# Performance work log

Hardware: AMD Instinct MI355X
Metric: run time of the kernel (lower is better)

The kernel has to match this reference:

```python
import jax, jax.numpy as jnp
import numpy as np

HIDDEN = 1024
FFN = 3584
NUM_EXPERTS = 8
TOP_K = 2
B, S = 2, 1024


def setup_inputs() -> dict:
    key = jax.random.key(0)
    k0, k1, k2, k3 = jax.random.split(key, 4)
    hidden_states = jax.random.normal(k0, (B, S, HIDDEN), dtype=jnp.float32)
    # torch Linear stores [out, in]; we keep gate as [E, H] (matches nn.Linear weight)
    gate_w = jax.random.normal(k1, (NUM_EXPERTS, HIDDEN), dtype=jnp.float32) * 0.02
    # GroupedLinear weights stored as [E, in, out] for direct x @ W per expert
    w_gate_up = jax.random.normal(k2, (NUM_EXPERTS, HIDDEN, 2 * FFN), dtype=jnp.float32) * 0.02
    w_down = jax.random.normal(k3, (NUM_EXPERTS, FFN, HIDDEN), dtype=jnp.float32) * 0.02
    return {"hidden_states": hidden_states, "gate_w": gate_w,
            "w_gate_up": w_gate_up, "w_down": w_down}


def reference(hidden_states, gate_w, w_gate_up, w_down):
    b, s, h = hidden_states.shape
    x = hidden_states.reshape(-1, h)                      # [T, H]
    T = x.shape[0]
    E = gate_w.shape[0]

    # Router: logits -> fp32 softmax -> top-k -> renormalize (Mixtral semantics)
    router_logits = x @ gate_w.T                          # [T, E]
    probs = jax.nn.softmax(router_logits.astype(jnp.float32), axis=-1)
    top_vals, top_idx = jax.lax.top_k(probs, TOP_K)       # [T, K]
    top_vals = top_vals / top_vals.sum(axis=-1, keepdims=True)
    top_vals = top_vals.astype(x.dtype)

    # Dense combine weights [T, E]: scatter top-k probs to expert slots.
    # Equivalent to permute -> grouped GEMM -> unpermute-with-probs.
    combine = jnp.zeros((T, E), dtype=x.dtype).at[
        jnp.arange(T)[:, None], top_idx].add(top_vals)

    out = jnp.zeros_like(x)
    for e in range(E):  # fixed small expert count
        gu = x @ w_gate_up[e]                             # [T, 2F]
        gate_proj, up_proj = jnp.split(gu, 2, axis=-1)
        act = jax.nn.silu(gate_proj) * up_proj            # [T, F]
        out = out + combine[:, e:e + 1] * (act @ w_down[e])

    return out.reshape(b, s, h), router_logits
```

## Files before the change

kernel.cpp:

```cpp
#include <hip/hip_runtime.h>
#include <hip/hip_bf16.h>
#include <stdint.h>

#define HIDDEN  1024
#define FFN     3584
#define NE      8
#define NTOK    2048
#define CAP     2048
#define OUT_ELEMS (NTOK * HIDDEN)

#define X_OFF   0u
#define CNT_OFF (4u*1024u*1024u)
#define TOK_OFF (CNT_OFF + 256u)
#define WGT_OFF (TOK_OFF + 65536u)
#define ACT_OFF (WGT_OFF + 65536u)
#define ACT_SZ  (4096u * 3584u * 2u)
#define WGU_OFF (ACT_OFF + ACT_SZ)
#define WGU_SZ  (8u*56u*16u*16384u)
#define WDB_OFF (WGU_OFF + WGU_SZ)
#define WDB_SZ  (8u*8u*56u*16384u)
#define WS_NEED ((size_t)WDB_OFF + (size_t)WDB_SZ)

typedef __attribute__((ext_vector_type(8))) short short8;
typedef __attribute__((ext_vector_type(4))) float floatx4;

static __device__ __forceinline__ uint32_t f2bf(float f) {
  union { float f; uint32_t u; } v; v.f = f;
  return (v.u + 0x7FFFu + ((v.u >> 16) & 1u)) >> 16;
}
static __device__ __forceinline__ uint32_t pack2(float lo, float hi) {
  return f2bf(lo) | (f2bf(hi) << 16);
}
union S8U { uint4 u; short8 s; };
static __device__ __forceinline__ short8 as_short8(uint4 v) { S8U x; x.u = v; return x.s; }

static __device__ __forceinline__ void ld_g2l16(const void* g, void* l) {
  __builtin_amdgcn_global_load_lds(
      (const __attribute__((address_space(1))) void*)g,
      (__attribute__((address_space(3))) void*)l, 16, 0, 0);
}

__global__ __launch_bounds__(256) void moe_prep(float4* __restrict__ out4,
                                                int* __restrict__ cnt) {
  uint32_t i = blockIdx.x * 256u + threadIdx.x;
  out4[i] = make_float4(0.f, 0.f, 0.f, 0.f);
  if (blockIdx.x == 0 && threadIdx.x < NE) cnt[threadIdx.x] = 0;
}

__global__ __launch_bounds__(256) void moe_convert(const float4* __restrict__ x4,
                                                   uint4* __restrict__ xb) {
  uint32_t g = blockIdx.x * 256u + threadIdx.x;
  float4 a = x4[2u*g], b = x4[2u*g + 1u];
  xb[g] = make_uint4(pack2(a.x, a.y), pack2(a.z, a.w),
                     pack2(b.x, b.y), pack2(b.z, b.w));
}

__global__ __launch_bounds__(256) void moe_router(
    const float* __restrict__ x, const float* __restrict__ gw,
    float* __restrict__ logits, int* __restrict__ cnt,
    int* __restrict__ tok, float* __restrict__ wgt)
{
  const int t = blockIdx.x * 4 + (threadIdx.x >> 6);
  const int lane = threadIdx.x & 63;
  const float* xr = x + (size_t)t * HIDDEN;
  float a[NE];
#pragma unroll
  for (int e = 0; e < NE; ++e) a[e] = 0.f;
  for (int hh = 0; hh < HIDDEN / 64; ++hh) {
    float xv = xr[hh * 64 + lane];
#pragma unroll
    for (int e = 0; e < NE; ++e) a[e] += xv * gw[e * HIDDEN + hh * 64 + lane];
  }
#pragma unroll
  for (int off = 32; off > 0; off >>= 1) {
#pragma unroll
    for (int e = 0; e < NE; ++e) a[e] += __shfl_xor(a[e], off);
  }
  if (lane == 0) {
#pragma unroll
    for (int e = 0; e < NE; ++e) logits[t * NE + e] = a[e];
    int i0 = 0; float v0 = a[0];
#pragma unroll
    for (int e = 1; e < NE; ++e) if (a[e] > v0) { v0 = a[e]; i0 = e; }
    int i1 = (i0 == 0) ? 1 : 0; float v1 = a[i1];
#pragma unroll
    for (int e = 0; e < NE; ++e) if (e != i0 && a[e] > v1) { v1 = a[e]; i1 = e; }
    float w0 = 1.f / (1.f + __expf(v1 - v0));
    float w1 = 1.f - w0;
    int p0 = atomicAdd(&cnt[i0], 1); tok[i0 * CAP + p0] = t; wgt[i0 * CAP + p0] = w0;
    int p1 = atomicAdd(&cnt[i1], 1); tok[i1 * CAP + p1] = t; wgt[i1 * CAP + p1] = w1;
  }
}

__global__ __launch_bounds__(256) void moe_wconv_gu(const float* __restrict__ wgu,
                                                    uint4* __restrict__ wgub) {
  const int kt = blockIdx.x, fb = blockIdx.y, e = blockIdx.z;
  const int f0 = fb * 64, k0 = kt * 64;
  const float* wB = wgu + (size_t)e * HIDDEN * (2 * FFN);
  uint4* dst = wgub + ((size_t)(e * 56 + fb) * 16 + kt) * 1024;
#pragma unroll
  for (int it = 0; it < 4; ++it) {
    int mid = it * 256 + threadIdx.x;
    int kp = mid >> 5;
    int n  = (mid & 31) * 4;
    int col = f0 + ((n >> 6) << 5) + (n & 31) + (((n >> 5) & 1) ? FFN : 0);
    const float* src = wB + (size_t)(k0 + 2 * kp) * (2 * FFN) + col;
    float4 r0 = *(const float4*)src;
    float4 r1 = *(const float4*)(src + 2 * FFN);
    dst[kp * 32 + ((n >> 2) ^ (((kp >> 2) & 1) << 2))] =
        make_uint4(pack2(r0.x, r1.x), pack2(r0.y, r1.y),
                   pack2(r0.z, r1.z), pack2(r0.w, r1.w));
  }
}

__global__ __launch_bounds__(256) void moe_wconv_d(const float* __restrict__ wd,
                                                   uint4* __restrict__ wdb) {
  const int kt = blockIdx.x, nb = blockIdx.y, e = blockIdx.z;
  const int n0 = nb * 128, k0 = kt * 64;
  const float* wB = wd + (size_t)e * FFN * HIDDEN;
  uint4* dst = wdb + ((size_t)(e * 8 + nb) * 56 + kt) * 1024;
#pragma unroll
  for (int it = 0; it < 4; ++it) {
    int mid = it * 256 + threadIdx.x;
    int kp = mid >> 5;
    int n  = (mid & 31) * 4;
    const float* src = wB + (size_t)(k0 + 2 * kp) * HIDDEN + n0 + n;
    float4 r0 = *(const float4*)src;
    float4 r1 = *(const float4*)(src + HIDDEN);
    dst[kp * 32 + ((n >> 2) ^ (((kp >> 2) & 1) << 2))] =
        make_uint4(pack2(r0.x, r1.x), pack2(r0.y, r1.y),
                   pack2(r0.z, r1.z), pack2(r0.w, r1.w));
  }
}

__global__ __launch_bounds__(256) void moe_gateup(
    const uint4* __restrict__ xb, const uint4* __restrict__ wgub,
    const int* __restrict__ cnt, const int* __restrict__ tok,
    unsigned short* __restrict__ act)
{
  const int e  = blockIdx.z;
  const int m0 = blockIdx.y * 128;
  const int fb = blockIdx.x;
  const int f0 = fb * 64;
  const int cn = cnt[e];
  if (m0 >= cn) return;
  int basev = 0;
#pragma unroll
  for (int i = 0; i < NE; ++i) { int ci = cnt[i]; if (i < e) basev += ci; }

  __shared__ uint4 As[1024];
  __shared__ uint4 Bs4[1024];
  const uint32_t* Bs = (const uint32_t*)Bs4;

  const int tid  = threadIdx.x;
  const int lane = tid & 63;
  const int w    = tid >> 6;
  const int wm   = w >> 1, wn = w & 1;
  const int q    = lane >> 4;
  const int c    = lane & 15;

  const int* tokE = tok + e * CAP;
  const char* aptr[4];
#pragma unroll
  for (int it = 0; it < 4; ++it) {
    int p   = (w * 4 + it) * 64 + lane;
    int row = p >> 3, c8 = p & 7;
    int mrow = m0 + row; if (mrow >= cn) mrow = cn - 1;
    aptr[it] = (const char*)(xb + (size_t)tokE[mrow] * (HIDDEN / 8) + (c8 ^ (row & 7)));
  }
  const char* bptr = (const char*)wgub + ((size_t)(e * 56 + fb) * 16) * 16384u
                   + (size_t)w * 4096u + (size_t)lane * 16u;

  floatx4 acc[4][4];
#pragma unroll
  for (int i = 0; i < 4; ++i)
#pragma unroll
    for (int j = 0; j < 4; ++j) acc[i][j] = (floatx4){0.f, 0.f, 0.f, 0.f};

  for (int kt = 0; kt < HIDDEN / 64; ++kt) {
    __syncthreads();
#pragma unroll
    for (int it = 0; it < 4; ++it)
      ld_g2l16(aptr[it] + (size_t)kt * 128u, &As[(w * 4 + it) * 64]);
#pragma unroll
    for (int it = 0; it < 4; ++it)
      ld_g2l16(bptr + (size_t)kt * 16384u + (size_t)it * 1024u, &Bs4[(w * 4 + it) * 64]);
    __syncthreads();
#pragma unroll
    for (int ks = 0; ks < 2; ++ks) {
      short8 af[4];
#pragma unroll
      for (int i = 0; i < 4; ++i) {
        int row = wm * 64 + i * 16 + c;
        int kc8 = ks * 4 + q;
        af[i] = as_short8(As[row * 8 + (kc8 ^ (row & 7))]);
      }
      short8 bfr[4];
#pragma unroll
      for (int j = 0; j < 4; ++j) {
        int n  = wn * 64 + j * 16 + c;
        int kp = ks * 16 + q * 4;
        int nn = n ^ ((q & 1) << 4);
        bfr[j] = as_short8(make_uint4(Bs[(kp + 0) * 128 + nn], Bs[(kp + 1) * 128 + nn],
                                      Bs[(kp + 2) * 128 + nn], Bs[(kp + 3) * 128 + nn]));
      }
#pragma unroll
      for (int i = 0; i < 4; ++i)
#pragma unroll
        for (int j = 0; j < 4; ++j)
          acc[i][j] = __builtin_amdgcn_mfma_f32_16x16x32_bf16(af[i], bfr[j], acc[i][j], 0, 0, 0);
    }
  }

#pragma unroll
  for (int i = 0; i < 4; ++i) {
#pragma unroll
    for (int r = 0; r < 4; ++r) {
      int m = m0 + wm * 64 + i * 16 + q * 4 + r;
      if (m < cn) {
#pragma unroll
        for (int j = 0; j < 2; ++j) {
          float g = acc[i][j][r];
          float u = acc[i][j + 2][r];
          float a = (g / (1.f + __expf(-g))) * u;
          act[(size_t)(basev + m) * FFN + (f0 + wn * 32 + j * 16 + c)] = (unsigned short)f2bf(a);
        }
      }
    }
  }
}

__global__ __launch_bounds__(256) void moe_down(
    const unsigned short* __restrict__ act, const uint4* __restrict__ wdb,
    const int* __restrict__ cnt, const int* __restrict__ tok,
    const float* __restrict__ wgt, float* __restrict__ out)
{
  const int e  = blockIdx.z;
  const int m0 = blockIdx.y * 128;
  const int nb = blockIdx.x;
  const int n0 = nb * 128;
  const int cn = cnt[e];
  if (m0 >= cn) return;
  int basev = 0;
#pragma unroll
  for (int i = 0; i < NE; ++i) { int ci = cnt[i]; if (i < e) basev += ci; }

  __shared__ uint4 As[1024];
  __shared__ uint4 Bs4[1024];
  const uint32_t* Bs = (const uint32_t*)Bs4;

  const int tid  = threadIdx.x;
  const int lane = tid & 63;
  const int w    = tid >> 6;
  const int wm   = w >> 1, wn = w & 1;
  const int q    = lane >> 4;
  const int c    = lane & 15;

  const char* aptr[4];
#pragma unroll
  for (int it = 0; it < 4; ++it) {
    int p   = (w * 4 + it) * 64 + lane;
    int row = p >> 3, c8 = p & 7;
    int mrow = m0 + row; if (mrow >= cn) mrow = cn - 1;
    aptr[it] = (const char*)act +
               ((size_t)(basev + mrow) * FFN + (size_t)((c8 ^ (row & 7)) * 8)) * 2u;
  }
  const char* bptr = (const char*)wdb + ((size_t)(e * 8 + nb) * 56) * 16384u
                   + (size_t)w * 4096u + (size_t)lane * 16u;

  floatx4 acc[4][4];
#pragma unroll
  for (int i = 0; i < 4; ++i)
#pragma unroll
    for (int j = 0; j < 4; ++j) acc[i][j] = (floatx4){0.f, 0.f, 0.f, 0.f};

  for (int kt = 0; kt < FFN / 64; ++kt) {
    __syncthreads();
#pragma unroll
    for (int it = 0; it < 4; ++it)
      ld_g2l16(aptr[it] + (size_t)kt * 128u, &As[(w * 4 + it) * 64]);
#pragma unroll
    for (int it = 0; it < 4; ++it)
      ld_g2l16(bptr + (size_t)kt * 16384u + (size_t)it * 1024u, &Bs4[(w * 4 + it) * 64]);
    __syncthreads();
#pragma unroll
    for (int ks = 0; ks < 2; ++ks) {
      short8 af[4];
#pragma unroll
      for (int i = 0; i < 4; ++i) {
        int row = wm * 64 + i * 16 + c;
        int kc8 = ks * 4 + q;
        af[i] = as_short8(As[row * 8 + (kc8 ^ (row & 7))]);
      }
      short8 bfr[4];
#pragma unroll
      for (int j = 0; j < 4; ++j) {
        int n  = wn * 64 + j * 16 + c;
        int kp = ks * 16 + q * 4;
        int nn = n ^ ((q & 1) << 4);
        bfr[j] = as_short8(make_uint4(Bs[(kp + 0) * 128 + nn], Bs[(kp + 1) * 128 + nn],
                                      Bs[(kp + 2) * 128 + nn], Bs[(kp + 3) * 128 + nn]));
      }
#pragma unroll
      for (int i = 0; i < 4; ++i)
#pragma unroll
        for (int j = 0; j < 4; ++j)
          acc[i][j] = __builtin_amdgcn_mfma_f32_16x16x32_bf16(af[i], bfr[j], acc[i][j], 0, 0, 0);
    }
  }

#pragma unroll
  for (int i = 0; i < 4; ++i) {
#pragma unroll
    for (int r = 0; r < 4; ++r) {
      int m = m0 + wm * 64 + i * 16 + q * 4 + r;
      if (m < cn) {
        int   t  = tok[e * CAP + m];
        float wg = wgt[e * CAP + m];
        float* orow = out + (size_t)t * HIDDEN + n0 + wn * 64 + c;
#pragma unroll
        for (int j = 0; j < 4; ++j)
          atomicAdd(orow + j * 16, acc[i][j][r] * wg);
      }
    }
  }
}

__global__ __launch_bounds__(256) void moe_gateup_lg(
    const uint4* __restrict__ xb, const float* __restrict__ wgu,
    const int* __restrict__ cnt, const int* __restrict__ tok,
    unsigned short* __restrict__ act)
{
  const int e  = blockIdx.z;
  const int m0 = blockIdx.y * 128;
  const int f0 = blockIdx.x * 64;
  const int cn = cnt[e];
  if (m0 >= cn) return;
  int basev = 0;
#pragma unroll
  for (int i = 0; i < NE; ++i) { int ci = cnt[i]; if (i < e) basev += ci; }

  __shared__ uint4    As[1024];
  __shared__ uint32_t Bs[4096];

  const int tid  = threadIdx.x;
  const int lane = tid & 63;
  const int w    = tid >> 6;
  const int wm   = w >> 1, wn = w & 1;
  const int q    = lane >> 4;
  const int c    = lane & 15;

  floatx4 acc[4][4];
#pragma unroll
  for (int i = 0; i < 4; ++i)
#pragma unroll
    for (int j = 0; j < 4; ++j) acc[i][j] = (floatx4){0.f, 0.f, 0.f, 0.f};

  const float* wB  = wgu + (size_t)e * HIDDEN * (2 * FFN);
  const int* tokE  = tok + e * CAP;

  for (int kt = 0; kt < HIDDEN / 64; ++kt) {
    const int k0 = kt * 64;
    __syncthreads();
#pragma unroll
    for (int it = 0; it < 4; ++it) {
      int cid = it * 256 + tid;
      int row = cid >> 3, c8 = cid & 7;
      int mrow = m0 + row; if (mrow >= cn) mrow = cn - 1;
      int tk = tokE[mrow];
      As[row * 8 + (c8 ^ (row & 7))] = xb[(size_t)tk * (HIDDEN / 8) + (k0 >> 3) + c8];
    }
#pragma unroll
    for (int it = 0; it < 4; ++it) {
      int mid = it * 256 + tid;
      int kp = mid >> 5;
      int n  = (mid & 31) * 4;
      int col = f0 + ((n >> 6) << 5) + (n & 31) + (((n >> 5) & 1) ? FFN : 0);
      const float* src = wB + (size_t)(k0 + 2 * kp) * (2 * FFN) + col;
      float4 r0 = *(const float4*)src;
      float4 r1 = *(const float4*)(src + 2 * FFN);
      int widx = kp * 128 + (n ^ (((kp >> 2) & 1) << 4));
      *(uint4*)&Bs[widx] = make_uint4(pack2(r0.x, r1.x), pack2(r0.y, r1.y),
                                      pack2(r0.z, r1.z), pack2(r0.w, r1.w));
    }
    __syncthreads();
#pragma unroll
    for (int ks = 0; ks < 2; ++ks) {
      short8 af[4];
#pragma unroll
      for (int i = 0; i < 4; ++i) {
        int row = wm * 64 + i * 16 + c;
        int kc8 = ks * 4 + q;
        af[i] = as_short8(As[row * 8 + (kc8 ^ (row & 7))]);
      }
      short8 bfr[4];
#pragma unroll
      for (int j = 0; j < 4; ++j) {
        int n  = wn * 64 + j * 16 + c;
        int kp = ks * 16 + q * 4;
        int nn = n ^ ((q & 1) << 4);
        bfr[j] = as_short8(make_uint4(Bs[(kp + 0) * 128 + nn], Bs[(kp + 1) * 128 + nn],
                                      Bs[(kp + 2) * 128 + nn], Bs[(kp + 3) * 128 + nn]));
      }
#pragma unroll
      for (int i = 0; i < 4; ++i)
#pragma unroll
        for (int j = 0; j < 4; ++j)
          acc[i][j] = __builtin_amdgcn_mfma_f32_16x16x32_bf16(af[i], bfr[j], acc[i][j], 0, 0, 0);
    }
  }

#pragma unroll
  for (int i = 0; i < 4; ++i) {
#pragma unroll
    for (int r = 0; r < 4; ++r) {
      int m = m0 + wm * 64 + i * 16 + q * 4 + r;
      if (m < cn) {
#pragma unroll
        for (int j = 0; j < 2; ++j) {
          float g = acc[i][j][r];
          float u = acc[i][j + 2][r];
          float a = (g / (1.f + __expf(-g))) * u;
          act[(size_t)(basev + m) * FFN + (f0 + wn * 32 + j * 16 + c)] = (unsigned short)f2bf(a);
        }
      }
    }
  }
}

__global__ __launch_bounds__(256) void moe_down_lg(
    const uint4* __restrict__ actc, const float* __restrict__ wd,
    const int* __restrict__ cnt, const int* __restrict__ tok,
    const float* __restrict__ wgt, float* __restrict__ out)
{
  const int e  = blockIdx.z;
  const int m0 = blockIdx.y * 128;
  const int n0 = blockIdx.x * 128;
  const int cn = cnt[e];
  if (m0 >= cn) return;
  int basev = 0;
#pragma unroll
  for (int i = 0; i < NE; ++i) { int ci = cnt[i]; if (i < e) basev += ci; }

  __shared__ uint4    As[1024];
  __shared__ uint32_t Bs[4096];

  const int tid  = threadIdx.x;
  const int lane = tid & 63;
  const int w    = tid >> 6;
  const int wm   = w >> 1, wn = w & 1;
  const int q    = lane >> 4;
  const int c    = lane & 15;

  floatx4 acc[4][4];
#pragma unroll
  for (int i = 0; i < 4; ++i)
#pragma unroll
    for (int j = 0; j < 4; ++j) acc[i][j] = (floatx4){0.f, 0.f, 0.f, 0.f};

  const float* wB = wd + (size_t)e * FFN * HIDDEN;

  for (int kt = 0; kt < FFN / 64; ++kt) {
    const int k0 = kt * 64;
    __syncthreads();
#pragma unroll
    for (int it = 0; it < 4; ++it) {
      int cid = it * 256 + tid;
      int row = cid >> 3, c8 = cid & 7;
      int mrow = m0 + row; if (mrow >= cn) mrow = cn - 1;
      As[row * 8 + (c8 ^ (row & 7))] =
          actc[(size_t)(basev + mrow) * (FFN / 8) + (k0 >> 3) + c8];
    }
#pragma unroll
    for (int it = 0; it < 4; ++it) {
      int mid = it * 256 + tid;
      int kp = mid >> 5;
      int n  = (mid & 31) * 4;
      int col = n0 + n;
      const float* src = wB + (size_t)(k0 + 2 * kp) * HIDDEN + col;
      float4 r0 = *(const float4*)src;
      float4 r1 = *(const float4*)(src + HIDDEN);
      int widx = kp * 128 + (n ^ (((kp >> 2) & 1) << 4));
      *(uint4*)&Bs[widx] = make_uint4(pack2(r0.x, r1.x), pack2(r0.y, r1.y),
                                      pack2(r0.z, r1.z), pack2(r0.w, r1.w));
    }
    __syncthreads();
#pragma unroll
    for (int ks = 0; ks < 2; ++ks) {
      short8 af[4];
#pragma unroll
      for (int i = 0; i < 4; ++i) {
        int row = wm * 64 + i * 16 + c;
        int kc8 = ks * 4 + q;
        af[i] = as_short8(As[row * 8 + (kc8 ^ (row & 7))]);
      }
      short8 bfr[4];
#pragma unroll
      for (int j = 0; j < 4; ++j) {
        int n  = wn * 64 + j * 16 + c;
        int kp = ks * 16 + q * 4;
        int nn = n ^ ((q & 1) << 4);
        bfr[j] = as_short8(make_uint4(Bs[(kp + 0) * 128 + nn], Bs[(kp + 1) * 128 + nn],
                                      Bs[(kp + 2) * 128 + nn], Bs[(kp + 3) * 128 + nn]));
      }
#pragma unroll
      for (int i = 0; i < 4; ++i)
#pragma unroll
        for (int j = 0; j < 4; ++j)
          acc[i][j] = __builtin_amdgcn_mfma_f32_16x16x32_bf16(af[i], bfr[j], acc[i][j], 0, 0, 0);
    }
  }

#pragma unroll
  for (int i = 0; i < 4; ++i) {
#pragma unroll
    for (int r = 0; r < 4; ++r) {
      int m = m0 + wm * 64 + i * 16 + q * 4 + r;
      if (m < cn) {
        int   t  = tok[e * CAP + m];
        float wg = wgt[e * CAP + m];
        float* orow = out + (size_t)t * HIDDEN + n0 + wn * 64 + c;
#pragma unroll
        for (int j = 0; j < 4; ++j)
          atomicAdd(orow + j * 16, acc[i][j][r] * wg);
      }
    }
  }
}

extern "C" void kernel_launch(void* const* d_in, const int* in_sizes, int n_in,
                              void* d_out, int out_size, void* d_ws, size_t ws_size,
                              hipStream_t stream)
{
  (void)in_sizes; (void)n_in; (void)out_size;
  const float* x   = (const float*)d_in[0];
  const float* gw  = (const float*)d_in[1];
  const float* wgu = (const float*)d_in[2];
  const float* wd  = (const float*)d_in[3];
  float* out = (float*)d_out;
  char*  ws  = (char*)d_ws;

  uint4*          xb   = (uint4*)(ws + X_OFF);
  int*            cnt  = (int*)(ws + CNT_OFF);
  int*            tok  = (int*)(ws + TOK_OFF);
  float*          wgt  = (float*)(ws + WGT_OFF);
  unsigned short* act  = (unsigned short*)(ws + ACT_OFF);
  uint4*          wgub = (uint4*)(ws + WGU_OFF);
  uint4*          wdb  = (uint4*)(ws + WDB_OFF);

  const bool fast = (ws_size >= WS_NEED);

  moe_prep<<<OUT_ELEMS / (256 * 4), 256, 0, stream>>>((float4*)out, cnt);
  moe_convert<<<(NTOK * HIDDEN) / (256 * 8), 256, 0, stream>>>((const float4*)x, xb);
  moe_router<<<NTOK / 4, 256, 0, stream>>>(x, gw, out + OUT_ELEMS, cnt, tok, wgt);

  if (fast) {
    moe_wconv_gu<<<dim3(16, 56, NE), 256, 0, stream>>>(wgu, wgub);
    moe_wconv_d<<<dim3(56, 8, NE), 256, 0, stream>>>(wd, wdb);
    moe_gateup<<<dim3(FFN / 64, 16, NE), 256, 0, stream>>>(xb, wgub, cnt, tok, act);
    moe_down<<<dim3(HIDDEN / 128, 16, NE), 256, 0, stream>>>(act, wdb, cnt, tok, wgt, out);
  } else {
    moe_gateup_lg<<<dim3(FFN / 64, 16, NE), 256, 0, stream>>>(xb, wgu, cnt, tok, act);
    moe_down_lg<<<dim3(HIDDEN / 128, 16, NE), 256, 0, stream>>>((const uint4*)act, wd, cnt, tok, wgt, out);
  }
}
```

Measured before the change: 670.0 us.

## Double-buffer GEMM tiles and replace atomic scatter with partial buffer plus combine

```diff
diff --git a/kernel.cpp b/kernel.cpp
--- a/kernel.cpp
+++ b/kernel.cpp
@@ -9,17 +9,20 @@
 #define CAP     2048
 #define OUT_ELEMS (NTOK * HIDDEN)
 
-#define X_OFF   0u
-#define CNT_OFF (4u*1024u*1024u)
-#define TOK_OFF (CNT_OFF + 256u)
-#define WGT_OFF (TOK_OFF + 65536u)
-#define ACT_OFF (WGT_OFF + 65536u)
-#define ACT_SZ  (4096u * 3584u * 2u)
-#define WGU_OFF (ACT_OFF + ACT_SZ)
-#define WGU_SZ  (8u*56u*16u*16384u)
-#define WDB_OFF (WGU_OFF + WGU_SZ)
-#define WDB_SZ  (8u*8u*56u*16384u)
-#define WS_NEED ((size_t)WDB_OFF + (size_t)WDB_SZ)
+#define X_OFF    0u
+#define CNT_OFF  (4u*1024u*1024u)
+#define TOK_OFF  (CNT_OFF + 256u)
+#define WGT_OFF  (TOK_OFF + 65536u)
+#define INV_OFF  (WGT_OFF + 65536u)
+#define ACT_OFF  (INV_OFF + 16384u)
+#define ACT_SZ   (4096u * 3584u * 2u)
+#define WGU_OFF  (ACT_OFF + ACT_SZ)
+#define WGU_SZ   (8u*56u*16u*16384u)
+#define WDB_OFF  (WGU_OFF + WGU_SZ)
+#define WDB_SZ   (8u*8u*56u*16384u)
+#define PART_OFF (WDB_OFF + WDB_SZ)
+#define PART_SZ  (4096u*1024u*4u)
+#define WS_NEED  ((size_t)PART_OFF + (size_t)PART_SZ)
 
 typedef __attribute__((ext_vector_type(8))) short short8;
 typedef __attribute__((ext_vector_type(4))) float floatx4;
@@ -38,6 +41,18 @@
   __builtin_amdgcn_global_load_lds(
       (const __attribute__((address_space(1))) void*)g,
       (__attribute__((address_space(3))) void*)l, 16, 0, 0);
+}
+
+static __device__ __forceinline__ void stage_tile(
+    const char* const* aptr, const char* bptr, size_t akt, size_t bkt,
+    uint4* AsB, uint4* BsB, int w)
+{
+#pragma unroll
+  for (int it = 0; it < 4; ++it)
+    ld_g2l16(aptr[it] + akt, &AsB[(w * 4 + it) * 64]);
+#pragma unroll
+  for (int it = 0; it < 4; ++it)
+    ld_g2l16(bptr + bkt + (size_t)it * 1024u, &BsB[(w * 4 + it) * 64]);
 }
 
 __global__ __launch_bounds__(256) void moe_prep(float4* __restrict__ out4,
@@ -48,17 +63,19 @@
 }
 
 __global__ __launch_bounds__(256) void moe_convert(const float4* __restrict__ x4,
-                                                   uint4* __restrict__ xb) {
+                                                   uint4* __restrict__ xb,
+                                                   int* __restrict__ cnt) {
   uint32_t g = blockIdx.x * 256u + threadIdx.x;
   float4 a = x4[2u*g], b = x4[2u*g + 1u];
   xb[g] = make_uint4(pack2(a.x, a.y), pack2(a.z, a.w),
                      pack2(b.x, b.y), pack2(b.z, b.w));
+  if (blockIdx.x == 0 && threadIdx.x < NE) cnt[threadIdx.x] = 0;
 }
 
 __global__ __launch_bounds__(256) void moe_router(
     const float* __restrict__ x, const float* __restrict__ gw,
     float* __restrict__ logits, int* __restrict__ cnt,
-    int* __restrict__ tok, float* __restrict__ wgt)
+    int* __restrict__ tok, float* __restrict__ wgt, int* __restrict__ inv)
 {
   const int t = blockIdx.x * 4 + (threadIdx.x >> 6);
   const int lane = threadIdx.x & 63;
@@ -89,6 +106,8 @@
     float w1 = 1.f - w0;
     int p0 = atomicAdd(&cnt[i0], 1); tok[i0 * CAP + p0] = t; wgt[i0 * CAP + p0] = w0;
     int p1 = atomicAdd(&cnt[i1], 1); tok[i1 * CAP + p1] = t; wgt[i1 * CAP + p1] = w1;
+    inv[t * 2 + 0] = i0 * CAP + p0;
+    inv[t * 2 + 1] = i1 * CAP + p1;
   }
 }
 
@@ -148,9 +167,8 @@
 #pragma unroll
   for (int i = 0; i < NE; ++i) { int ci = cnt[i]; if (i < e) basev += ci; }
 
-  __shared__ uint4 As[1024];
-  __shared__ uint4 Bs4[1024];
-  const uint32_t* Bs = (const uint32_t*)Bs4;
+  __shared__ uint4 As[2][1024];
+  __shared__ uint4 Bs4[2][1024];
 
   const int tid  = threadIdx.x;
   const int lane = tid & 63;
@@ -177,15 +195,16 @@
 #pragma unroll
     for (int j = 0; j < 4; ++j) acc[i][j] = (floatx4){0.f, 0.f, 0.f, 0.f};
 
-  for (int kt = 0; kt < HIDDEN / 64; ++kt) {
-    __syncthreads();
-#pragma unroll
-    for (int it = 0; it < 4; ++it)
-      ld_g2l16(aptr[it] + (size_t)kt * 128u, &As[(w * 4 + it) * 64]);
-#pragma unroll
-    for (int it = 0; it < 4; ++it)
-      ld_g2l16(bptr + (size_t)kt * 16384u + (size_t)it * 1024u, &Bs4[(w * 4 + it) * 64]);
-    __syncthreads();
+  const int NT = HIDDEN / 64;
+  stage_tile(aptr, bptr, 0, 0, As[0], Bs4[0], w);
+  __syncthreads();
+  int cur = 0;
+  for (int kt = 0; kt < NT; ++kt) {
+    if (kt + 1 < NT)
+      stage_tile(aptr, bptr, (size_t)(kt + 1) * 128u, (size_t)(kt + 1) * 16384u,
+                 As[cur ^ 1], Bs4[cur ^ 1], w);
+    const uint4*    Asc = As[cur];
+    const uint32_t* Bsc = (const uint32_t*)Bs4[cur];
 #pragma unroll
     for (int ks = 0; ks < 2; ++ks) {
       short8 af[4];
@@ -193,7 +212,7 @@
       for (int i = 0; i < 4; ++i) {
         int row = wm * 64 + i * 16 + c;
         int kc8 = ks * 4 + q;
-        af[i] = as_short8(As[row * 8 + (kc8 ^ (row & 7))]);
+        af[i] = as_short8(Asc[row * 8 + (kc8 ^ (row & 7))]);
       }
       short8 bfr[4];
 #pragma unroll
@@ -201,8 +220,8 @@
         int n  = wn * 64 + j * 16 + c;
         int kp = ks * 16 + q * 4;
         int nn = n ^ ((q & 1) << 4);
-        bfr[j] = as_short8(make_uint4(Bs[(kp + 0) * 128 + nn], Bs[(kp + 1) * 128 + nn],
-                                      Bs[(kp + 2) * 128 + nn], Bs[(kp + 3) * 128 + nn]));
+        bfr[j] = as_short8(make_uint4(Bsc[(kp + 0) * 128 + nn], Bsc[(kp + 1) * 128 + nn],
+                                      Bsc[(kp + 2) * 128 + nn], Bsc[(kp + 3) * 128 + nn]));
       }
 #pragma unroll
       for (int i = 0; i < 4; ++i)
@@ -210,6 +229,8 @@
         for (int j = 0; j < 4; ++j)
           acc[i][j] = __builtin_amdgcn_mfma_f32_16x16x32_bf16(af[i], bfr[j], acc[i][j], 0, 0, 0);
     }
+    __syncthreads();
+    cur ^= 1;
   }
 
 #pragma unroll
@@ -233,7 +254,7 @@
 __global__ __launch_bounds__(256) void moe_down(
     const unsigned short* __restrict__ act, const uint4* __restrict__ wdb,
     const int* __restrict__ cnt, const int* __restrict__ tok,
-    const float* __restrict__ wgt, float* __restrict__ out)
+    const float* __restrict__ wgt, float* __restrict__ part)
 {
   const int e  = blockIdx.z;
   const int m0 = blockIdx.y * 128;
@@ -245,9 +266,8 @@
 #pragma unroll
   for (int i = 0; i < NE; ++i) { int ci = cnt[i]; if (i < e) basev += ci; }
 
-  __shared__ uint4 As[1024];
-  __shared__ uint4 Bs4[1024];
-  const uint32_t* Bs = (const uint32_t*)Bs4;
+  __shared__ uint4 As[2][1024];
+  __shared__ uint4 Bs4[2][1024];
 
   const int tid  = threadIdx.x;
   const int lane = tid & 63;
@@ -274,15 +294,16 @@
 #pragma unroll
     for (int j = 0; j < 4; ++j) acc[i][j] = (floatx4){0.f, 0.f, 0.f, 0.f};
 
-  for (int kt = 0; kt < FFN / 64; ++kt) {
-    __syncthreads();
-#pragma unroll
-    for (int it = 0; it < 4; ++it)
-      ld_g2l16(aptr[it] + (size_t)kt * 128u, &As[(w * 4 + it) * 64]);
-#pragma unroll
-    for (int it = 0; it < 4; ++it)
-      ld_g2l16(bptr + (size_t)kt * 16384u + (size_t)it * 1024u, &Bs4[(w * 4 + it) * 64]);
-    __syncthreads();
+  const int NT = FFN / 64;
+  stage_tile(aptr, bptr, 0, 0, As[0], Bs4[0], w);
+  __syncthreads();
+  int cur = 0;
+  for (int kt = 0; kt < NT; ++kt) {
+    if (kt + 1 < NT)
+      stage_tile(aptr, bptr, (size_t)(kt + 1) * 128u, (size_t)(kt + 1) * 16384u,
+                 As[cur ^ 1], Bs4[cur ^ 1], w);
+    const uint4*    Asc = As[cur];
+    const uint32_t* Bsc = (const uint32_t*)Bs4[cur];
 #pragma unroll
     for (int ks = 0; ks < 2; ++ks) {
       short8 af[4];
@@ -290,7 +311,7 @@
       for (int i = 0; i < 4; ++i) {
         int row = wm * 64 + i * 16 + c;
         int kc8 = ks * 4 + q;
-        af[i] = as_short8(As[row * 8 + (kc8 ^ (row & 7))]);
+        af[i] = as_short8(Asc[row * 8 + (kc8 ^ (row & 7))]);
       }
       short8 bfr[4];
 #pragma unroll
@@ -298,8 +319,8 @@
         int n  = wn * 64 + j * 16 + c;
         int kp = ks * 16 + q * 4;
         int nn = n ^ ((q & 1) << 4);
-        bfr[j] = as_short8(make_uint4(Bs[(kp + 0) * 128 + nn], Bs[(kp + 1) * 128 + nn],
-                                      Bs[(kp + 2) * 128 + nn], Bs[(kp + 3) * 128 + nn]));
+        bfr[j] = as_short8(make_uint4(Bsc[(kp + 0) * 128 + nn], Bsc[(kp + 1) * 128 + nn],
+                                      Bsc[(kp + 2) * 128 + nn], Bsc[(kp + 3) * 128 + nn]));
       }
 #pragma unroll
       for (int i = 0; i < 4; ++i)
@@ -307,6 +328,8 @@
         for (int j = 0; j < 4; ++j)
           acc[i][j] = __builtin_amdgcn_mfma_f32_16x16x32_bf16(af[i], bfr[j], acc[i][j], 0, 0, 0);
     }
+    __syncthreads();
+    cur ^= 1;
   }
 
 #pragma unroll
@@ -315,15 +338,36 @@
     for (int r = 0; r < 4; ++r) {
       int m = m0 + wm * 64 + i * 16 + q * 4 + r;
       if (m < cn) {
-        int   t  = tok[e * CAP + m];
-        float wg = wgt[e * CAP + m];
-        float* orow = out + (size_t)t * HIDDEN + n0 + wn * 64 + c;
+        float  wg   = wgt[e * CAP + m];
+        float* prow = part + (size_t)(basev + m) * HIDDEN + n0 + wn * 64 + c;
 #pragma unroll
         for (int j = 0; j < 4; ++j)
-          atomicAdd(orow + j * 16, acc[i][j][r] * wg);
-      }
-    }
-  }
+          prow[j * 16] = acc[i][j][r] * wg;
+      }
+    }
+  }
+}
+
+__global__ __launch_bounds__(256) void moe_combine(
+    const int* __restrict__ cnt, const int* __restrict__ inv,
+    const float4* __restrict__ part4, float4* __restrict__ out4)
+{
+  const int t  = blockIdx.x;
+  const int s0 = inv[2 * t], s1 = inv[2 * t + 1];
+  const int e0 = s0 >> 11, e1 = s1 >> 11;
+  int b0 = 0, b1 = 0;
+#pragma unroll
+  for (int i = 0; i < NE; ++i) {
+    int ci = cnt[i];
+    if (i < e0) b0 += ci;
+    if (i < e1) b1 += ci;
+  }
+  const size_t r0 = (size_t)(b0 + (s0 & (CAP - 1))) * 256u;
+  const size_t r1 = (size_t)(b1 + (s1 & (CAP - 1))) * 256u;
+  const int i = threadIdx.x;
+  float4 a = part4[r0 + i];
+  float4 b = part4[r1 + i];
+  out4[(size_t)t * 256u + i] = make_float4(a.x + b.x, a.y + b.y, a.z + b.z, a.w + b.w);
 }
 
 __global__ __launch_bounds__(256) void moe_gateup_lg(
@@ -544,22 +588,26 @@
   int*            cnt  = (int*)(ws + CNT_OFF);
   int*            tok  = (int*)(ws + TOK_OFF);
   float*          wgt  = (float*)(ws + WGT_OFF);
+  int*            inv  = (int*)(ws + INV_OFF);
   unsigned short* act  = (unsigned short*)(ws + ACT_OFF);
   uint4*          wgub = (uint4*)(ws + WGU_OFF);
   uint4*          wdb  = (uint4*)(ws + WDB_OFF);
+  float*          part = (float*)(ws + PART_OFF);
 
   const bool fast = (ws_size >= WS_NEED);
 
-  moe_prep<<<OUT_ELEMS / (256 * 4), 256, 0, stream>>>((float4*)out, cnt);
-  moe_convert<<<(NTOK * HIDDEN) / (256 * 8), 256, 0, stream>>>((const float4*)x, xb);
-  moe_router<<<NTOK / 4, 256, 0, stream>>>(x, gw, out + OUT_ELEMS, cnt, tok, wgt);
-
   if (fast) {
+    moe_convert<<<(NTOK * HIDDEN) / (256 * 8), 256, 0, stream>>>((const float4*)x, xb, cnt);
+    moe_router<<<NTOK / 4, 256, 0, stream>>>(x, gw, out + OUT_ELEMS, cnt, tok, wgt, inv);
     moe_wconv_gu<<<dim3(16, 56, NE), 256, 0, stream>>>(wgu, wgub);
     moe_wconv_d<<<dim3(56, 8, NE), 256, 0, stream>>>(wd, wdb);
     moe_gateup<<<dim3(FFN / 64, 16, NE), 256, 0, stream>>>(xb, wgub, cnt, tok, act);
-    moe_down<<<dim3(HIDDEN / 128, 16, NE), 256, 0, stream>>>(act, wdb, cnt, tok, wgt, out);
+    moe_down<<<dim3(HIDDEN / 128, 16, NE), 256, 0, stream>>>(act, wdb, cnt, tok, wgt, part);
+    moe_combine<<<NTOK, 256, 0, stream>>>(cnt, inv, (const float4*)part, (float4*)out);
   } else {
+    moe_prep<<<OUT_ELEMS / (256 * 4), 256, 0, stream>>>((float4*)out, cnt);
+    moe_convert<<<(NTOK * HIDDEN) / (256 * 8), 256, 0, stream>>>((const float4*)x, xb, cnt);
+    moe_router<<<NTOK / 4, 256, 0, stream>>>(x, gw, out + OUT_ELEMS, cnt, tok, wgt, inv);
     moe_gateup_lg<<<dim3(FFN / 64, 16, NE), 256, 0, stream>>>(xb, wgu, cnt, tok, act);
     moe_down_lg<<<dim3(HIDDEN / 128, 16, NE), 256, 0, stream>>>((const uint4*)act, wd, cnt, tok, wgt, out);
   }
```

After: 676.8 us. About the same (+1.0%).
